# Kernel tuning notes

Measured on AMD Instinct MI355X. Metric: run time of the kernel, lower is better.

Reference implementation:

```python
import jax, jax.numpy as jnp
import numpy as np

EPS = 1e-8

def setup_inputs() -> dict:
    key = jax.random.key(0)
    k1, k2, k3 = jax.random.split(key, 3)
    B, N, L = 4096, 8192, 256
    logits = jax.random.normal(k1, (B, N), dtype=jnp.float32)
    positive_ids = jax.random.randint(k2, (B, L), 0, N, dtype=jnp.int64)
    positive_weights = jax.random.uniform(k3, (B, L), dtype=jnp.float32)
    return {"logits": logits, "positive_ids": positive_ids, "positive_weights": positive_weights}

def reference(logits, positive_ids, positive_weights):
    # gather positive logits: [B, L]
    gathered = jnp.take_along_axis(logits, positive_ids, axis=1)
    w = positive_weights.astype(jnp.float32)
    w = w / jnp.maximum(w.sum(axis=-1, keepdims=True), EPS)
    # sort by weight descending
    order = jnp.argsort(-w, axis=-1)
    ordered_logits = jnp.take_along_axis(gathered, order, axis=1)
    ordered_weights = jnp.take_along_axis(w, order, axis=1)
    # suffix logsumexp in one reverse cumulative pass: [B, L]
    suffix_lse = jax.lax.cumlogsumexp(ordered_logits, axis=1, reverse=True)
    listmle = jnp.sum(ordered_weights * (suffix_lse - ordered_logits), axis=-1)
    return jnp.mean(listmle)
```

## Files before the change

kernel.cpp:

```cpp
#include <hip/hip_runtime.h>
#include <hip/hip_bf16.h>
#include <math.h>

#define BROWS 4096
#define NCOLS 8192
#define LLEN  256
#define EPSV  1e-8f

__global__ void zero_out_kernel(float* out) { out[0] = 0.0f; }

__global__ __launch_bounds__(256) void listmle_kernel(
    const float* __restrict__ logits,
    const int*   __restrict__ ids,
    const float* __restrict__ weights,
    float*       __restrict__ out)
{
    __shared__ float s_g[LLEN];
    __shared__ unsigned long long s_key[2][LLEN];
    __shared__ float s_aggm[4], s_aggs[4];
    __shared__ float s_redt[4], s_redw[4];

    const int tid  = threadIdx.x;
    const int lane = tid & 63;
    const int wv   = tid >> 6;
    const int b    = blockIdx.x;

    float w  = weights[(size_t)b * LLEN + tid];
    int   id = ids[(size_t)b * LLEN + tid];
    float g  = logits[(size_t)b * NCOLS + id];
    s_g[tid] = g;

    unsigned key_hi = __float_as_uint(w);
    unsigned key_lo = (unsigned)(LLEN - 1 - tid);

    int phase = 0;
    #pragma unroll
    for (int k = 2; k <= LLEN; k <<= 1) {
        #pragma unroll
        for (int j = k >> 1; j > 0; j >>= 1) {
            const bool keep_max = (((tid & k) == 0) == ((tid & j) == 0));
            unsigned p_hi, p_lo;
            if (j < 64) {
                p_hi = __shfl_xor(key_hi, j);
                p_lo = __shfl_xor(key_lo, j);
            } else {
                s_key[phase][tid] = ((unsigned long long)key_hi << 32) | key_lo;
                __syncthreads();
                unsigned long long p = s_key[phase][tid ^ j];
                p_hi = (unsigned)(p >> 32);
                p_lo = (unsigned)p;
                phase ^= 1;
            }
            const bool pgt  = (p_hi > key_hi) || (p_hi == key_hi && p_lo > key_lo);
            if (pgt == keep_max) { key_hi = p_hi; key_lo = p_lo; }
        }
    }

    float ow  = __uint_as_float(key_hi);
    int   pos = (LLEN - 1) - (int)key_lo;
    float og  = s_g[pos];

    float m = og, s = 1.0f;
    #pragma unroll
    for (int off = 1; off < 64; off <<= 1) {
        float mp = __shfl_down(m, off);
        float sp = __shfl_down(s, off);
        if (lane + off < 64) {
            float nm = fmaxf(m, mp);
            s = s * __expf(m - nm) + sp * __expf(mp - nm);
            m = nm;
        }
    }
    if (lane == 0) { s_aggm[wv] = m; s_aggs[wv] = s; }
    __syncthreads();
    #pragma unroll
    for (int w2 = 0; w2 < 4; ++w2) {
        if (w2 > wv) {
            float mp = s_aggm[w2], sp = s_aggs[w2];
            float nm = fmaxf(m, mp);
            s = s * __expf(m - nm) + sp * __expf(mp - nm);
            m = nm;
        }
    }
    float suffix_lse = m + logf(s);

    float t  = ow * (suffix_lse - og);
    float ws = ow;
    #pragma unroll
    for (int o = 32; o > 0; o >>= 1) {
        t  += __shfl_down(t, o);
        ws += __shfl_down(ws, o);
    }
    if (lane == 0) { s_redt[wv] = t; s_redw[wv] = ws; }
    __syncthreads();
    if (tid == 0) {
        float tot  = s_redt[0] + s_redt[1] + s_redt[2] + s_redt[3];
        float wsum = s_redw[0] + s_redw[1] + s_redw[2] + s_redw[3];
        float loss = tot / fmaxf(wsum, EPSV);
        atomicAdd(out, loss * (1.0f / (float)BROWS));
    }
}

extern "C" void kernel_launch(void* const* d_in, const int* in_sizes, int n_in,
                              void* d_out, int out_size, void* d_ws, size_t ws_size,
                              hipStream_t stream) {
    const float* logits  = (const float*)d_in[0];
    const int*   ids     = (const int*)d_in[1];
    const float* weights = (const float*)d_in[2];
    float* out = (float*)d_out;

    zero_out_kernel<<<dim3(1), dim3(1), 0, stream>>>(out);
    listmle_kernel<<<dim3(BROWS), dim3(LLEN), 0, stream>>>(logits, ids, weights, out);
}
```

Before: 220.7 us.

## Sort each row in one wavefront with four keys per lane and packed keys

Each row is now handled by a single 64-lane wavefront that holds four elements per lane. The 64-bit sort key becomes a 32-bit key: the weight's top 24 bits plus an 8-bit index. Bitonic steps run in registers and through cross-lane shuffles, with no shared-memory barriers, and the suffix logsumexp becomes a per-lane serial scan followed by a wave scan. The global atomic accumulation is replaced by per-row partials and a last-block reduction, and the zero kernel is replaced by a memset. Truncating the low mantissa bits can change the order of weights that are nearly equal, which slightly changes the sort semantics.

```diff
diff --git a/kernel.cpp b/kernel.cpp
--- a/kernel.cpp
+++ b/kernel.cpp
@@ -6,98 +6,144 @@
 #define NCOLS 8192
 #define LLEN  256
 #define EPSV  1e-8f
+#define NEG_BIG -3.0e38f
 
-__global__ void zero_out_kernel(float* out) { out[0] = 0.0f; }
+__device__ __forceinline__ void lse_combine(float& m, float& s, float mo, float so) {
+    float nm = fmaxf(m, mo);
+    s = s * __expf(m - nm) + so * __expf(mo - nm);
+    m = nm;
+}
 
-__global__ __launch_bounds__(256) void listmle_kernel(
+__global__ __launch_bounds__(64) void listmle_kernel(
     const float* __restrict__ logits,
     const int*   __restrict__ ids,
     const float* __restrict__ weights,
+    float*       __restrict__ partial,
+    unsigned*    __restrict__ counter,
     float*       __restrict__ out)
 {
     __shared__ float s_g[LLEN];
-    __shared__ unsigned long long s_key[2][LLEN];
-    __shared__ float s_aggm[4], s_aggs[4];
-    __shared__ float s_redt[4], s_redw[4];
+    __shared__ float s_w[LLEN];
+    __shared__ int   s_last;
 
-    const int tid  = threadIdx.x;
-    const int lane = tid & 63;
-    const int wv   = tid >> 6;
+    const int lane = threadIdx.x;
     const int b    = blockIdx.x;
 
-    float w  = weights[(size_t)b * LLEN + tid];
-    int   id = ids[(size_t)b * LLEN + tid];
-    float g  = logits[(size_t)b * NCOLS + id];
-    s_g[tid] = g;
+    const int base = b * LLEN + 4 * lane;
+    const int4   id4 = *(const int4*)(ids + base);
+    const float4 w4  = *(const float4*)(weights + base);
+    const float* row = logits + (size_t)b * NCOLS;
+    float g0 = row[id4.x], g1 = row[id4.y], g2 = row[id4.z], g3 = row[id4.w];
 
-    unsigned key_hi = __float_as_uint(w);
-    unsigned key_lo = (unsigned)(LLEN - 1 - tid);
+    float wr[4] = {w4.x, w4.y, w4.z, w4.w};
+    unsigned key[4];
+    #pragma unroll
+    for (int r = 0; r < 4; ++r)
+        key[r] = (__float_as_uint(wr[r]) & 0xFFFFFF00u)
+               | (unsigned)(LLEN - 1 - (4 * lane + r));
 
-    int phase = 0;
     #pragma unroll
     for (int k = 2; k <= LLEN; k <<= 1) {
         #pragma unroll
         for (int j = k >> 1; j > 0; j >>= 1) {
-            const bool keep_max = (((tid & k) == 0) == ((tid & j) == 0));
-            unsigned p_hi, p_lo;
-            if (j < 64) {
-                p_hi = __shfl_xor(key_hi, j);
-                p_lo = __shfl_xor(key_lo, j);
+            if (j >= 4) {
+                const int jl = j >> 2;
+                #pragma unroll
+                for (int r = 0; r < 4; ++r) {
+                    const int i = 4 * lane + r;
+                    const bool keep_max = (((i & k) == 0) == ((i & j) == 0));
+                    unsigned p  = __shfl_xor(key[r], jl);
+                    unsigned mx = key[r] > p ? key[r] : p;
+                    unsigned mn = key[r] > p ? p : key[r];
+                    key[r] = keep_max ? mx : mn;
+                }
+            } else if (j == 2) {
+                #pragma unroll
+                for (int ra = 0; ra < 2; ++ra) {
+                    const int rb = ra + 2;
+                    const int i  = 4 * lane + ra;
+                    const bool km = ((i & k) == 0);
+                    unsigned a = key[ra], c = key[rb];
+                    unsigned mx = a > c ? a : c, mn = a > c ? c : a;
+                    key[ra] = km ? mx : mn;
+                    key[rb] = km ? mn : mx;
+                }
             } else {
-                s_key[phase][tid] = ((unsigned long long)key_hi << 32) | key_lo;
-                __syncthreads();
-                unsigned long long p = s_key[phase][tid ^ j];
-                p_hi = (unsigned)(p >> 32);
-                p_lo = (unsigned)p;
-                phase ^= 1;
+                #pragma unroll
+                for (int ra = 0; ra < 4; ra += 2) {
+                    const int rb = ra + 1;
+                    const int i  = 4 * lane + ra;
+                    const bool km = ((i & k) == 0);
+                    unsigned a = key[ra], c = key[rb];
+                    unsigned mx = a > c ? a : c, mn = a > c ? c : a;
+                    key[ra] = km ? mx : mn;
+                    key[rb] = km ? mn : mx;
+                }
             }
-            const bool pgt  = (p_hi > key_hi) || (p_hi == key_hi && p_lo > key_lo);
-            if (pgt == keep_max) { key_hi = p_hi; key_lo = p_lo; }
         }
     }
 
-    float ow  = __uint_as_float(key_hi);
-    int   pos = (LLEN - 1) - (int)key_lo;
-    float og  = s_g[pos];
+    *(float4*)(s_g + 4 * lane) = make_float4(g0, g1, g2, g3);
+    *(float4*)(s_w + 4 * lane) = make_float4(wr[0], wr[1], wr[2], wr[3]);
+    __syncthreads();
 
-    float m = og, s = 1.0f;
+    float og[4], ow[4];
+    #pragma unroll
+    for (int r = 0; r < 4; ++r) {
+        const int pos = (LLEN - 1) - (int)(key[r] & 0xFFu);
+        og[r] = s_g[pos];
+        ow[r] = s_w[pos];
+    }
+
+    float sm[4], ss[4];
+    sm[3] = og[3]; ss[3] = 1.0f;
+    #pragma unroll
+    for (int r = 2; r >= 0; --r) {
+        sm[r] = og[r]; ss[r] = 1.0f;
+        lse_combine(sm[r], ss[r], sm[r + 1], ss[r + 1]);
+    }
+    float Am = sm[0], As = ss[0];
     #pragma unroll
     for (int off = 1; off < 64; off <<= 1) {
-        float mp = __shfl_down(m, off);
-        float sp = __shfl_down(s, off);
-        if (lane + off < 64) {
-            float nm = fmaxf(m, mp);
-            s = s * __expf(m - nm) + sp * __expf(mp - nm);
-            m = nm;
-        }
+        float pm = __shfl_down(Am, off);
+        float ps = __shfl_down(As, off);
+        if (lane + off < 64) lse_combine(Am, As, pm, ps);
     }
-    if (lane == 0) { s_aggm[wv] = m; s_aggs[wv] = s; }
-    __syncthreads();
+    float Em = __shfl_down(Am, 1);
+    float Es = __shfl_down(As, 1);
+    if (lane == 63) { Em = NEG_BIG; Es = 0.0f; }
+
+    float t = 0.0f, ws = 0.0f;
     #pragma unroll
-    for (int w2 = 0; w2 < 4; ++w2) {
-        if (w2 > wv) {
-            float mp = s_aggm[w2], sp = s_aggs[w2];
-            float nm = fmaxf(m, mp);
-            s = s * __expf(m - nm) + sp * __expf(mp - nm);
-            m = nm;
-        }
+    for (int r = 0; r < 4; ++r) {
+        float m = sm[r], s = ss[r];
+        lse_combine(m, s, Em, Es);
+        t  += ow[r] * ((m + __logf(s)) - og[r]);
+        ws += ow[r];
     }
-    float suffix_lse = m + logf(s);
-
-    float t  = ow * (suffix_lse - og);
-    float ws = ow;
     #pragma unroll
     for (int o = 32; o > 0; o >>= 1) {
         t  += __shfl_down(t, o);
         ws += __shfl_down(ws, o);
     }
-    if (lane == 0) { s_redt[wv] = t; s_redw[wv] = ws; }
+
+    if (lane == 0) {
+        partial[b] = t / fmaxf(ws, EPSV);
+        __threadfence();
+        unsigned old = atomicAdd(counter, 1u);
+        s_last = (old == BROWS - 1) ? 1 : 0;
+    }
     __syncthreads();
-    if (tid == 0) {
-        float tot  = s_redt[0] + s_redt[1] + s_redt[2] + s_redt[3];
-        float wsum = s_redw[0] + s_redw[1] + s_redw[2] + s_redw[3];
-        float loss = tot / fmaxf(wsum, EPSV);
-        atomicAdd(out, loss * (1.0f / (float)BROWS));
+    if (s_last) {
+        __threadfence();
+        float v = 0.0f;
+        #pragma unroll
+        for (int i = 0; i < BROWS / 64; ++i)
+            v += __hip_atomic_load(&partial[i * 64 + lane],
+                                   __ATOMIC_RELAXED, __HIP_MEMORY_SCOPE_AGENT);
+        #pragma unroll
+        for (int o = 32; o > 0; o >>= 1) v += __shfl_down(v, o);
+        if (lane == 0) out[0] = v * (1.0f / (float)BROWS);
     }
 }
 
@@ -107,8 +153,11 @@
     const float* logits  = (const float*)d_in[0];
     const int*   ids     = (const int*)d_in[1];
     const float* weights = (const float*)d_in[2];
-    float* out = (float*)d_out;
+    float*    out     = (float*)d_out;
+    float*    partial = (float*)d_ws;
+    unsigned* counter = (unsigned*)d_ws + BROWS;
 
-    zero_out_kernel<<<dim3(1), dim3(1), 0, stream>>>(out);
-    listmle_kernel<<<dim3(BROWS), dim3(LLEN), 0, stream>>>(logits, ids, weights, out);
+    hipMemsetAsync(counter, 0, sizeof(unsigned), stream);
+    listmle_kernel<<<dim3(BROWS), dim3(64), 0, stream>>>(
+        logits, ids, weights, partial, counter, out);
 }
```

Measured after the change: 344.5 us. 56.1% more time.
